# Optimization experiments

Hardware: AMD Instinct MI355X
Metric: run time of the kernel (lower is better)

The kernel has to match this reference:

```python
import jax, jax.numpy as jnp
import numpy as np

NQ = 8    # QCNN qubits
NLQ = 4   # QLSTM qubits == hidden_dim
C64 = jnp.complex64

H_GATE = (1.0 / np.sqrt(2.0)) * jnp.array([[1, 1], [1, -1]], dtype=C64)


def ap1(st, U, q):
    # apply 2x2 gate U on qubit axis q of state st (shape (2,)*n)
    s = jnp.moveaxis(st, q, -1)
    s = jnp.einsum('ij,...j->...i', U, s)
    return jnp.moveaxis(s, -1, q)


def apcx(st, c, t):
    # CNOT with control c, target t: flip target slice where control == 1
    s = jnp.moveaxis(st, (c, t), (-2, -1))
    s = jnp.stack([s[..., 0, :], s[..., 1, ::-1]], axis=-2)
    return jnp.moveaxis(s, (-2, -1), (c, t))


def RX(t):
    c = jnp.cos(t / 2).astype(C64)
    s = (-1j * jnp.sin(t / 2)).astype(C64)
    return jnp.stack([jnp.stack([c, s]), jnp.stack([s, c])])


def RY(t):
    c = jnp.cos(t / 2)
    s = jnp.sin(t / 2)
    return jnp.stack([jnp.stack([c, -s]), jnp.stack([s, c])]).astype(C64)


def RZ(t):
    e = jnp.exp(-0.5j * t).astype(C64)
    z = jnp.zeros((), C64)
    return jnp.stack([jnp.stack([e, z]), jnp.stack([z, jnp.conj(e)])])


def PH(t):
    # qiskit phase gate P(t) = diag(1, e^{i t})
    e = jnp.exp(1j * t).astype(C64)
    o = jnp.ones((), C64)
    z = jnp.zeros((), C64)
    return jnp.stack([jnp.stack([o, z]), jnp.stack([z, e])])


def init_state(n):
    st = jnp.zeros((2,) * n, C64)
    return st.at[(0,) * n].set(1.0)


def zexp(st, q):
    # <Z_q> of statevector st
    p = st.real ** 2 + st.imag ** 2
    m = p.sum(axis=tuple(a for a in range(st.ndim) if a != q))
    return m[0] - m[1]


def conv_block(st, p, q1, q2):
    st = ap1(st, RZ(-np.pi / 2), q2)
    st = apcx(st, q2, q1)
    st = ap1(st, RZ(p[0]), q1)
    st = ap1(st, RY(p[1]), q2)
    st = apcx(st, q1, q2)
    st = ap1(st, RY(p[2]), q2)
    st = apcx(st, q2, q1)
    st = ap1(st, RZ(np.pi / 2), q1)
    return st


def pool_block(st, p, src, sink):
    st = ap1(st, RZ(-np.pi / 2), sink)
    st = apcx(st, sink, src)
    st = ap1(st, RZ(p[0]), src)
    st = ap1(st, RY(p[1]), sink)
    st = apcx(st, src, sink)
    st = ap1(st, RY(p[2]), sink)
    return st


QCNN_SPECS = [
    (conv_block, [(0, 1), (2, 3), (4, 5), (6, 7)]),  # c1
    (pool_block, [(0, 1), (2, 3), (4, 5), (6, 7)]),  # p1
    (conv_block, [(0, 1), (2, 3)]),                  # c2
    (pool_block, [(0, 1), (2, 3)]),                  # p2
    (conv_block, [(0, 1)]),                          # c3
    (pool_block, [(0, 1)]),                          # p3
]


def qcnn_single(x, w):
    # x: (8,) feature angles, w: (42,) ansatz weights
    st = init_state(NQ)
    for _ in range(2):
        for q in range(NQ):
            st = ap1(st, H_GATE, q)
        for q in range(NQ):
            st = ap1(st, PH(2.0 * x[q]), q)
    idx = 0
    for blk, prs in QCNN_SPECS:
        for a, b in prs:
            st = blk(st, w[idx:idx + 3], a, b)
            idx += 3
    return zexp(st, NQ - 1)  # 'ZIIIIIII' => Z on qubit 7 (little-endian)


def qgate_single(v, theta):
    # v: (4,) encoder angles (per sample), theta: (4,) trainable RX angles
    st = init_state(NLQ)
    for i in range(NLQ):
        st = ap1(st, RX(v[i]), i)
    for i in range(NLQ):
        st = ap1(st, RX(theta[i]), i)
    for i in range(NLQ - 1):
        st = apcx(st, i, i + 1)
    st = apcx(st, NLQ - 1, 0)
    return jnp.stack([zexp(st, q) for q in range(NLQ)])


qgate = jax.vmap(qgate_single, in_axes=(0, None))


def setup_inputs() -> dict:
    key = jax.random.key(0)
    ks = jax.random.split(key, 12)
    B, S = 16, 128
    x = jax.random.uniform(ks[0], (B, S, NQ), jnp.float32) * np.pi
    qcnn_w = jax.random.normal(ks[1], (42,), jnp.float32) * 0.1

    def lin(k, out_d, in_d):
        k1, k2 = jax.random.split(k)
        lim = 1.0 / np.sqrt(in_d)
        W = jax.random.uniform(k1, (out_d, in_d), jnp.float32, -lim, lim)
        b = jax.random.uniform(k2, (out_d,), jnp.float32, -lim, lim)
        return W, b

    Wf, bf = lin(ks[2], NLQ, 1 + NLQ)
    Wi, bi = lin(ks[3], NLQ, 1 + NLQ)
    Wg, bg = lin(ks[4], NLQ, 1 + NLQ)
    Wo, bo = lin(ks[5], NLQ, 1 + NLQ)
    theta_f = jax.random.normal(ks[6], (NLQ,), jnp.float32) * 0.1
    theta_i = jax.random.normal(ks[7], (NLQ,), jnp.float32) * 0.1
    theta_g = jax.random.normal(ks[8], (NLQ,), jnp.float32) * 0.1
    theta_o = jax.random.normal(ks[9], (NLQ,), jnp.float32) * 0.1
    Wh, bh = lin(ks[10], 1, NLQ)
    return dict(x=x, qcnn_w=qcnn_w, theta_f=theta_f, theta_i=theta_i,
                theta_g=theta_g, theta_o=theta_o, Wf=Wf, bf=bf, Wi=Wi, bi=bi,
                Wg=Wg, bg=bg, Wo=Wo, bo=bo, Wh=Wh, bh=bh)


def reference(x, qcnn_w, theta_f, theta_i, theta_g, theta_o,
              Wf, bf, Wi, bi, Wg, bg, Wo, bo, Wh, bh):
    B, S, _ = x.shape
    flat = x.reshape(B * S, NQ)
    qcnn_out = jax.vmap(qcnn_single, in_axes=(0, None))(flat, qcnn_w)
    qcnn_out = qcnn_out.reshape(B, S, 1)
    lstm_in = jnp.transpose(qcnn_out, (1, 0, 2))  # (S, B, 1)
    h0 = jnp.zeros((B, NLQ), x.dtype)
    c0 = jnp.zeros((B, NLQ), x.dtype)

    def step(carry, xt):
        hx, cx = carry
        comb = jnp.concatenate([xt, hx], axis=1)  # (B, 1 + hidden)
        f = jax.nn.sigmoid(qgate(comb @ Wf.T + bf, theta_f))
        i = jax.nn.sigmoid(qgate(comb @ Wi.T + bi, theta_i))
        g = jnp.tanh(qgate(comb @ Wg.T + bg, theta_g))
        o = jax.nn.sigmoid(qgate(comb @ Wo.T + bo, theta_o))
        cx = f * cx + i * g
        hx = o * jnp.tanh(cx)
        return (hx, cx), hx

    _, outs = jax.lax.scan(step, (h0, c0), lstm_in)  # outs: (S, B, hidden)
    logits = outs[-1] @ Wh.T + bh  # (B, 1)
    return qcnn_out, logits
```

## Files before the change

kernel.cpp:

```cpp
#include <hip/hip_runtime.h>
#include <math.h>

#define PI_F 3.14159265358979323846f
#define FLAG_MAGIC 0x9E3779B9u

typedef int v2i __attribute__((ext_vector_type(2)));

__device__ __forceinline__ float rcpf(float x) { return __builtin_amdgcn_rcpf(x); }
__device__ __forceinline__ void fswap(float2& p, float2& q) { float2 t = p; p = q; q = t; }


template<int Q>
__device__ __forceinline__ float exq(float v) {
    if constexpr (Q == 2)
        return __int_as_float(__builtin_amdgcn_update_dpp(0, __float_as_int(v), 0xB1, 0xF, 0xF, true));
    else if constexpr (Q == 3)
        return __int_as_float(__builtin_amdgcn_update_dpp(0, __float_as_int(v), 0x4E, 0xF, 0xF, true));
    else if constexpr (Q == 4)
        return __int_as_float(__builtin_amdgcn_ds_swizzle(__float_as_int(v), 0x101F));
    else if constexpr (Q == 5)
        return __int_as_float(__builtin_amdgcn_ds_swizzle(__float_as_int(v), 0x201F));
    else if constexpr (Q == 6)
        return __int_as_float(__builtin_amdgcn_ds_swizzle(__float_as_int(v), 0x401F));
    else {
        v2i r = __builtin_amdgcn_permlane32_swap(__float_as_int(v), __float_as_int(v), false, false);
        return __int_as_float((threadIdx.x & 32) ? r[0] : r[1]);
    }
}

template<int Q>
__device__ __forceinline__ void rzg(float2 a[4], float th, int lane) {
    float c = __cosf(0.5f * th), s = __sinf(0.5f * th);
    if constexpr (Q >= 2) {
        float se = ((lane >> (Q - 2)) & 1) ? s : -s;
        #pragma unroll
        for (int r = 0; r < 4; ++r) {
            float nx = c * a[r].x - se * a[r].y;
            float ny = c * a[r].y + se * a[r].x;
            a[r] = make_float2(nx, ny);
        }
    } else {
        #pragma unroll
        for (int r = 0; r < 4; ++r) {
            int bit = (Q == 0) ? (r >> 1) : (r & 1);
            float se = bit ? s : -s;
            float nx = c * a[r].x - se * a[r].y;
            float ny = c * a[r].y + se * a[r].x;
            a[r] = make_float2(nx, ny);
        }
    }
}

template<int Q>
__device__ __forceinline__ void ryg(float2 a[4], float th, int lane) {
    float c = __cosf(0.5f * th), s = __sinf(0.5f * th);
    if constexpr (Q >= 2) {
        float se = ((lane >> (Q - 2)) & 1) ? s : -s;
        #pragma unroll
        for (int r = 0; r < 4; ++r) {
            float ox = exq<Q>(a[r].x), oy = exq<Q>(a[r].y);
            a[r] = make_float2(c * a[r].x + se * ox, c * a[r].y + se * oy);
        }
    } else if constexpr (Q == 0) {
        #pragma unroll
        for (int r = 0; r < 2; ++r) {
            float2 lo = a[r], hi = a[r + 2];
            a[r]     = make_float2(c * lo.x - s * hi.x, c * lo.y - s * hi.y);
            a[r + 2] = make_float2(s * lo.x + c * hi.x, s * lo.y + c * hi.y);
        }
    } else {
        #pragma unroll
        for (int r = 0; r < 4; r += 2) {
            float2 lo = a[r], hi = a[r + 1];
            a[r]     = make_float2(c * lo.x - s * hi.x, c * lo.y - s * hi.y);
            a[r + 1] = make_float2(s * lo.x + c * hi.x, s * lo.y + c * hi.y);
        }
    }
}

template<int C, int T>
__device__ __forceinline__ void cxg(float2 a[4], int lane) {
    if constexpr (C >= 2) {
        bool cb = (lane >> (C - 2)) & 1;
        #pragma unroll
        for (int r = 0; r < 4; ++r) {
            float ox = exq<T>(a[r].x), oy = exq<T>(a[r].y);
            a[r].x = cb ? ox : a[r].x;
            a[r].y = cb ? oy : a[r].y;
        }
    } else if constexpr (C == 0 && T == 1) {
        fswap(a[2], a[3]);
    } else {
        fswap(a[1], a[3]);
    }
}

template<int Q>
__device__ __forceinline__ void featg(float2 a[4], float xq, int lane) {
    float phi = 2.0f * xq;
    float e1x = __cosf(phi), e1y = __sinf(phi);
    float e2x = e1x * e1x - e1y * e1y;
    float e2y = 2.0f * e1x * e1y;
    float2 u00 = make_float2(0.5f * (1.0f + e1x),  0.5f * e1y);
    float2 u01 = make_float2(0.5f * (1.0f - e1x), -0.5f * e1y);
    float2 u10 = make_float2(0.5f * (e1x - e2x), 0.5f * (e1y - e2y));
    float2 u11 = make_float2(0.5f * (e1x + e2x), 0.5f * (e1y + e2y));
    if constexpr (Q >= 2) {
        bool bset = (lane >> (Q - 2)) & 1;
        float csx = bset ? u11.x : u00.x, csy = bset ? u11.y : u00.y;
        float cox = bset ? u10.x : u01.x, coy = bset ? u10.y : u01.y;
        #pragma unroll
        for (int r = 0; r < 4; ++r) {
            float ox = exq<Q>(a[r].x), oy = exq<Q>(a[r].y);
            float nx = csx * a[r].x - csy * a[r].y + cox * ox - coy * oy;
            float ny = csx * a[r].y + csy * a[r].x + cox * oy + coy * ox;
            a[r] = make_float2(nx, ny);
        }
    } else {
        float2 l, h;
        #define APPL(LO, HI)                                                        \
            l = a[LO]; h = a[HI];                                                   \
            a[LO] = make_float2(u00.x*l.x - u00.y*l.y + u01.x*h.x - u01.y*h.y,      \
                                u00.x*l.y + u00.y*l.x + u01.x*h.y + u01.y*h.x);     \
            a[HI] = make_float2(u10.x*l.x - u10.y*l.y + u11.x*h.x - u11.y*h.y,      \
                                u10.x*l.y + u10.y*l.x + u11.x*h.y + u11.y*h.x);
        if constexpr (Q == 0) { APPL(0, 2) APPL(1, 3) }
        else                  { APPL(0, 1) APPL(2, 3) }
        #undef APPL
    }
}

template<int Q1, int Q2>
__device__ __forceinline__ void convg(float2 a[4], const float* __restrict__ p, int lane) {
    rzg<Q2>(a, -0.5f * PI_F, lane);
    cxg<Q2, Q1>(a, lane);
    rzg<Q1>(a, p[0], lane);
    ryg<Q2>(a, p[1], lane);
    cxg<Q1, Q2>(a, lane);
    ryg<Q2>(a, p[2], lane);
    cxg<Q2, Q1>(a, lane);
    rzg<Q1>(a, 0.5f * PI_F, lane);
}

template<int Q1, int Q2>
__device__ __forceinline__ void poolg(float2 a[4], const float* __restrict__ p, int lane) {
    rzg<Q2>(a, -0.5f * PI_F, lane);
    cxg<Q2, Q1>(a, lane);
    rzg<Q1>(a, p[0], lane);
    ryg<Q2>(a, p[1], lane);
    cxg<Q1, Q2>(a, lane);
    ryg<Q2>(a, p[2], lane);
}

template<int CTRL>
__device__ __forceinline__ float bq(float v) {
    return __int_as_float(__builtin_amdgcn_update_dpp(0, __float_as_int(v), CTRL, 0xF, 0xF, true));
}

__device__ __forceinline__ float pick4(bool b0, bool b1, float a0, float a1, float a2, float a3) {
    float t01 = b0 ? a1 : a0;
    float t23 = b0 ? a3 : a2;
    return b1 ? t23 : t01;
}


__global__ __launch_bounds__(256) void fused_kernel(
    const float* __restrict__ x,  const float* __restrict__ w,
    const float* __restrict__ thf, const float* __restrict__ thi,
    const float* __restrict__ thg, const float* __restrict__ tho,
    const float* __restrict__ Wf, const float* __restrict__ bf,
    const float* __restrict__ Wi, const float* __restrict__ bi,
    const float* __restrict__ Wg, const float* __restrict__ bg,
    const float* __restrict__ Wo, const float* __restrict__ bo,
    const float* __restrict__ Wh, const float* __restrict__ bh,
    float* __restrict__ out, unsigned long long* __restrict__ flg) {
    __shared__ __align__(16) float qsh[16 * 132];
    int lane = threadIdx.x & 63;
    int wave = threadIdx.x >> 6;
    unsigned* epoch = (unsigned*)(flg + 2048);

    if (blockIdx.x != 512) {
        unsigned key = FLAG_MAGIC ^ __hip_atomic_load(epoch, __ATOMIC_RELAXED, __HIP_MEMORY_SCOPE_AGENT);
        int n = blockIdx.x * 4 + wave;
        float2 a[4];
        a[0] = make_float2(lane == 0 ? 1.0f : 0.0f, 0.0f);
        a[1] = make_float2(0.0f, 0.0f);
        a[2] = make_float2(0.0f, 0.0f);
        a[3] = make_float2(0.0f, 0.0f);

        const float* xr = x + n * 8;
        featg<0>(a, xr[0], lane);
        featg<1>(a, xr[1], lane);
        featg<2>(a, xr[2], lane);
        featg<3>(a, xr[3], lane);
        featg<4>(a, xr[4], lane);
        featg<5>(a, xr[5], lane);
        featg<6>(a, xr[6], lane);
        featg<7>(a, xr[7], lane);

        convg<0,1>(a, w + 0,  lane);
        convg<2,3>(a, w + 3,  lane);
        convg<4,5>(a, w + 6,  lane);
        convg<6,7>(a, w + 9,  lane);
        poolg<0,1>(a, w + 12, lane);
        poolg<2,3>(a, w + 15, lane);
        poolg<4,5>(a, w + 18, lane);
        poolg<6,7>(a, w + 21, lane);
        convg<0,1>(a, w + 24, lane);
        convg<2,3>(a, w + 27, lane);
        poolg<0,1>(a, w + 30, lane);
        poolg<2,3>(a, w + 33, lane);
        convg<0,1>(a, w + 36, lane);
        poolg<0,1>(a, w + 39, lane);

        float ssum = 0.f;
        #pragma unroll
        for (int r = 0; r < 4; ++r)
            ssum += a[r].x * a[r].x + a[r].y * a[r].y;
        ssum = (lane & 32) ? -ssum : ssum;
        ssum += exq<2>(ssum);
        ssum += exq<3>(ssum);
        ssum += exq<4>(ssum);
        ssum += exq<5>(ssum);
        ssum += exq<6>(ssum);
        {
            v2i rr = __builtin_amdgcn_permlane32_swap(__float_as_int(ssum), __float_as_int(ssum), false, false);
            ssum = __int_as_float((threadIdx.x & 32) ? rr[0] : rr[1]) +
                   __int_as_float((threadIdx.x & 32) ? rr[1] : rr[0]);
        }
        if (lane == 0) {
            out[n] = ssum;
            unsigned long long pk = ((unsigned long long)__float_as_uint(ssum) << 32)
                                  | (unsigned long long)key;
            __hip_atomic_store(&flg[n], pk, __ATOMIC_RELAXED, __HIP_MEMORY_SCOPE_AGENT);
        }
        return;
    }

    if (wave != 0) return;
    unsigned key = FLAG_MAGIC ^ __hip_atomic_load(epoch, __ATOMIC_RELAXED, __HIP_MEMORY_SCOPE_AGENT);

    for (int j = 0; j < 32; ++j) {
        int idx = j * 64 + lane;
        unsigned long long v;
        do {
            v = __hip_atomic_load(&flg[idx], __ATOMIC_RELAXED, __HIP_MEMORY_SCOPE_AGENT);
        } while ((unsigned)v != key);
        qsh[(idx >> 7) * 132 + (idx & 127)] = __uint_as_float((unsigned)(v >> 32));
    }
    __builtin_amdgcn_wave_barrier();

    int b = lane >> 2, q = lane & 3;
    bool qb0 = q & 1, qb1 = q & 2;
    const float* Wp = (q == 0) ? Wf : (q == 1) ? Wi : (q == 2) ? Wg : Wo;
    const float* bp = (q == 0) ? bf : (q == 1) ? bi : (q == 2) ? bg : bo;
    const float* tp = (q == 0) ? thf : (q == 1) ? thi : (q == 2) ? thg : tho;

    float W[20], av[4];
    #pragma unroll
    for (int k = 0; k < 20; ++k) W[k] = Wp[k];
    #pragma unroll
    for (int r = 0; r < 4; ++r) av[r] = bp[r] + tp[r];

    float nA = (q == 2) ? 1.0f : 0.0f;
    float nB = (q == 2) ? -2.0f : 1.0f;
    float nK = (q == 2) ? 2.0f : -1.0f;

    float c = 0.f;
    float h0 = 0.f, h1 = 0.f, h2 = 0.f, h3 = 0.f;
    const float* qrow = &qsh[b * 132];
    float xv = qrow[0];

    for (int t = 0; t < 128; ++t) {
        float xn = qrow[t + 1];
        float vA = av[0] + W[0]*xv  + W[1]*h0  + W[2]*h1  + W[3]*h2  + W[4]*h3;
        float vB = av[1] + W[5]*xv  + W[6]*h0  + W[7]*h1  + W[8]*h2  + W[9]*h3;
        float vC = av[2] + W[10]*xv + W[11]*h0 + W[12]*h1 + W[13]*h2 + W[14]*h3;
        float vD = av[3] + W[15]*xv + W[16]*h0 + W[17]*h1 + W[18]*h2 + W[19]*h3;
        float cA = __cosf(vA), cB = __cosf(vB), cC = __cosf(vC), cD = __cosf(vD);
        float r1 = cA * cB, r2 = r1 * cC, r3 = r2 * cD, r0 = cB * (cC * cD);
        float E0 = __expf(nK * r0), E1 = __expf(nK * r1);
        float E2 = __expf(nK * r2), E3 = __expf(nK * r3);
        float n0 = nA + nB * rcpf(E0 + 1.0f);
        float n1 = nA + nB * rcpf(E1 + 1.0f);
        float n2 = nA + nB * rcpf(E2 + 1.0f);
        float n3 = nA + nB * rcpf(E3 + 1.0f);
        float F0 = bq<0x00>(n0), F1 = bq<0x00>(n1), F2 = bq<0x00>(n2), F3 = bq<0x00>(n3);
        float I0 = bq<0x55>(n0), I1 = bq<0x55>(n1), I2 = bq<0x55>(n2), I3 = bq<0x55>(n3);
        float G0 = bq<0xAA>(n0), G1 = bq<0xAA>(n1), G2 = bq<0xAA>(n2), G3 = bq<0xAA>(n3);
        float O0 = bq<0xFF>(n0), O1 = bq<0xFF>(n1), O2 = bq<0xFF>(n2), O3 = bq<0xFF>(n3);
        float F = pick4(qb0, qb1, F0, F1, F2, F3);
        float I = pick4(qb0, qb1, I0, I1, I2, I3);
        float G = pick4(qb0, qb1, G0, G1, G2, G3);
        float O = pick4(qb0, qb1, O0, O1, O2, O3);
        c = F * c + I * G;
        float Ec = __expf(2.0f * c);
        float tau = 1.0f - 2.0f * rcpf(Ec + 1.0f);
        float hq = O * tau;
        h0 = bq<0x00>(hq);
        h1 = bq<0x55>(hq);
        h2 = bq<0xAA>(hq);
        h3 = bq<0xFF>(hq);
        xv = xn;
    }

    if (q == 0)
        out[2048 + b] = bh[0] + Wh[0]*h0 + Wh[1]*h1 + Wh[2]*h2 + Wh[3]*h3;

    if (lane == 0)
        __hip_atomic_fetch_add(epoch, 1u, __ATOMIC_RELAXED, __HIP_MEMORY_SCOPE_AGENT);
}

extern "C" void kernel_launch(void* const* d_in, const int* in_sizes, int n_in,
                              void* d_out, int out_size, void* d_ws, size_t ws_size,
                              hipStream_t stream) {
    fused_kernel<<<513, 256, 0, stream>>>(
        (const float*)d_in[0],  (const float*)d_in[1],
        (const float*)d_in[2],  (const float*)d_in[3],
        (const float*)d_in[4],  (const float*)d_in[5],
        (const float*)d_in[6],  (const float*)d_in[7],
        (const float*)d_in[8],  (const float*)d_in[9],
        (const float*)d_in[10], (const float*)d_in[11],
        (const float*)d_in[12], (const float*)d_in[13],
        (const float*)d_in[14], (const float*)d_in[15],
        (float*)d_out, (unsigned long long*)d_ws);
}
```

Before: 129.3 us.

## Overlap LSTM recurrence with QCNN production via timestep-major flag ordering

QCNN work items are remapped so that flag index n is timestep-major (batch = n&15, t = n>>4). The LSTM wave can then consume 64-entry chunks covering four timesteps for all 16 batches as soon as they are ready, instead of waiting for all 2048 flags before starting the recurrence. Polling now uses s_sleep and is interleaved with the sequential scan loop. The risk is that the recurrence stalls whenever producer blocks are late, and that launch_bounds(256,1) changes occupancy for the QCNN blocks.

New measurement: 122.6 us. 1.05x faster.

```diff
diff --git a/kernel.cpp b/kernel.cpp
--- a/kernel.cpp
+++ b/kernel.cpp
@@ -164,7 +164,19 @@
 }
 
 
-__global__ __launch_bounds__(256) void fused_kernel(
+__device__ __forceinline__ void stage_chunk(int m, int lane, unsigned key,
+                                            unsigned long long* __restrict__ flg,
+                                            float* qsh) {
+    int idx = m * 64 + lane;
+    unsigned long long v = __hip_atomic_load(&flg[idx], __ATOMIC_RELAXED, __HIP_MEMORY_SCOPE_AGENT);
+    while ((unsigned)v != key) {
+        __builtin_amdgcn_s_sleep(1);
+        v = __hip_atomic_load(&flg[idx], __ATOMIC_RELAXED, __HIP_MEMORY_SCOPE_AGENT);
+    }
+    qsh[(idx & 15) * 132 + (idx >> 4)] = __uint_as_float((unsigned)(v >> 32));
+}
+
+__global__ __launch_bounds__(256, 1) void fused_kernel(
     const float* __restrict__ x,  const float* __restrict__ w,
     const float* __restrict__ thf, const float* __restrict__ thi,
     const float* __restrict__ thg, const float* __restrict__ tho,
@@ -182,13 +194,15 @@
     if (blockIdx.x != 512) {
         unsigned key = FLAG_MAGIC ^ __hip_atomic_load(epoch, __ATOMIC_RELAXED, __HIP_MEMORY_SCOPE_AGENT);
         int n = blockIdx.x * 4 + wave;
+        int bb = n & 15, tt = n >> 4;
+        int sidx = bb * 128 + tt;
         float2 a[4];
         a[0] = make_float2(lane == 0 ? 1.0f : 0.0f, 0.0f);
         a[1] = make_float2(0.0f, 0.0f);
         a[2] = make_float2(0.0f, 0.0f);
         a[3] = make_float2(0.0f, 0.0f);
 
-        const float* xr = x + n * 8;
+        const float* xr = x + sidx * 8;
         featg<0>(a, xr[0], lane);
         featg<1>(a, xr[1], lane);
         featg<2>(a, xr[2], lane);
@@ -229,7 +243,7 @@
                    __int_as_float((threadIdx.x & 32) ? rr[1] : rr[0]);
         }
         if (lane == 0) {
-            out[n] = ssum;
+            out[sidx] = ssum;
             unsigned long long pk = ((unsigned long long)__float_as_uint(ssum) << 32)
                                   | (unsigned long long)key;
             __hip_atomic_store(&flg[n], pk, __ATOMIC_RELAXED, __HIP_MEMORY_SCOPE_AGENT);
@@ -240,14 +254,7 @@
     if (wave != 0) return;
     unsigned key = FLAG_MAGIC ^ __hip_atomic_load(epoch, __ATOMIC_RELAXED, __HIP_MEMORY_SCOPE_AGENT);
 
-    for (int j = 0; j < 32; ++j) {
-        int idx = j * 64 + lane;
-        unsigned long long v;
-        do {
-            v = __hip_atomic_load(&flg[idx], __ATOMIC_RELAXED, __HIP_MEMORY_SCOPE_AGENT);
-        } while ((unsigned)v != key);
-        qsh[(idx >> 7) * 132 + (idx & 127)] = __uint_as_float((unsigned)(v >> 32));
-    }
+    stage_chunk(0, lane, key, flg, qsh);
     __builtin_amdgcn_wave_barrier();
 
     int b = lane >> 2, q = lane & 3;
@@ -269,39 +276,43 @@
     float c = 0.f;
     float h0 = 0.f, h1 = 0.f, h2 = 0.f, h3 = 0.f;
     const float* qrow = &qsh[b * 132];
-    float xv = qrow[0];
-
-    for (int t = 0; t < 128; ++t) {
-        float xn = qrow[t + 1];
-        float vA = av[0] + W[0]*xv  + W[1]*h0  + W[2]*h1  + W[3]*h2  + W[4]*h3;
-        float vB = av[1] + W[5]*xv  + W[6]*h0  + W[7]*h1  + W[8]*h2  + W[9]*h3;
-        float vC = av[2] + W[10]*xv + W[11]*h0 + W[12]*h1 + W[13]*h2 + W[14]*h3;
-        float vD = av[3] + W[15]*xv + W[16]*h0 + W[17]*h1 + W[18]*h2 + W[19]*h3;
-        float cA = __cosf(vA), cB = __cosf(vB), cC = __cosf(vC), cD = __cosf(vD);
-        float r1 = cA * cB, r2 = r1 * cC, r3 = r2 * cD, r0 = cB * (cC * cD);
-        float E0 = __expf(nK * r0), E1 = __expf(nK * r1);
-        float E2 = __expf(nK * r2), E3 = __expf(nK * r3);
-        float n0 = nA + nB * rcpf(E0 + 1.0f);
-        float n1 = nA + nB * rcpf(E1 + 1.0f);
-        float n2 = nA + nB * rcpf(E2 + 1.0f);
-        float n3 = nA + nB * rcpf(E3 + 1.0f);
-        float F0 = bq<0x00>(n0), F1 = bq<0x00>(n1), F2 = bq<0x00>(n2), F3 = bq<0x00>(n3);
-        float I0 = bq<0x55>(n0), I1 = bq<0x55>(n1), I2 = bq<0x55>(n2), I3 = bq<0x55>(n3);
-        float G0 = bq<0xAA>(n0), G1 = bq<0xAA>(n1), G2 = bq<0xAA>(n2), G3 = bq<0xAA>(n3);
-        float O0 = bq<0xFF>(n0), O1 = bq<0xFF>(n1), O2 = bq<0xFF>(n2), O3 = bq<0xFF>(n3);
-        float F = pick4(qb0, qb1, F0, F1, F2, F3);
-        float I = pick4(qb0, qb1, I0, I1, I2, I3);
-        float G = pick4(qb0, qb1, G0, G1, G2, G3);
-        float O = pick4(qb0, qb1, O0, O1, O2, O3);
-        c = F * c + I * G;
-        float Ec = __expf(2.0f * c);
-        float tau = 1.0f - 2.0f * rcpf(Ec + 1.0f);
-        float hq = O * tau;
-        h0 = bq<0x00>(hq);
-        h1 = bq<0x55>(hq);
-        h2 = bq<0xAA>(hq);
-        h3 = bq<0xFF>(hq);
-        xv = xn;
+
+    for (int j = 0; j < 32; ++j) {
+        if (j < 31) stage_chunk(j + 1, lane, key, flg, qsh);
+        __builtin_amdgcn_wave_barrier();
+        #pragma unroll
+        for (int k = 0; k < 4; ++k) {
+            int t = 4 * j + k;
+            float xv = qrow[t];
+            float vA = av[0] + W[0]*xv  + W[1]*h0  + W[2]*h1  + W[3]*h2  + W[4]*h3;
+            float vB = av[1] + W[5]*xv  + W[6]*h0  + W[7]*h1  + W[8]*h2  + W[9]*h3;
+            float vC = av[2] + W[10]*xv + W[11]*h0 + W[12]*h1 + W[13]*h2 + W[14]*h3;
+            float vD = av[3] + W[15]*xv + W[16]*h0 + W[17]*h1 + W[18]*h2 + W[19]*h3;
+            float cA = __cosf(vA), cB = __cosf(vB), cC = __cosf(vC), cD = __cosf(vD);
+            float r1 = cA * cB, r2 = r1 * cC, r3 = r2 * cD, r0 = cB * (cC * cD);
+            float E0 = __expf(nK * r0), E1 = __expf(nK * r1);
+            float E2 = __expf(nK * r2), E3 = __expf(nK * r3);
+            float n0 = nA + nB * rcpf(E0 + 1.0f);
+            float n1 = nA + nB * rcpf(E1 + 1.0f);
+            float n2 = nA + nB * rcpf(E2 + 1.0f);
+            float n3 = nA + nB * rcpf(E3 + 1.0f);
+            float F0 = bq<0x00>(n0), F1 = bq<0x00>(n1), F2 = bq<0x00>(n2), F3 = bq<0x00>(n3);
+            float I0 = bq<0x55>(n0), I1 = bq<0x55>(n1), I2 = bq<0x55>(n2), I3 = bq<0x55>(n3);
+            float G0 = bq<0xAA>(n0), G1 = bq<0xAA>(n1), G2 = bq<0xAA>(n2), G3 = bq<0xAA>(n3);
+            float O0 = bq<0xFF>(n0), O1 = bq<0xFF>(n1), O2 = bq<0xFF>(n2), O3 = bq<0xFF>(n3);
+            float F = pick4(qb0, qb1, F0, F1, F2, F3);
+            float I = pick4(qb0, qb1, I0, I1, I2, I3);
+            float G = pick4(qb0, qb1, G0, G1, G2, G3);
+            float O = pick4(qb0, qb1, O0, O1, O2, O3);
+            c = F * c + I * G;
+            float Ec = __expf(2.0f * c);
+            float tau = 1.0f - 2.0f * rcpf(Ec + 1.0f);
+            float hq = O * tau;
+            h0 = bq<0x00>(hq);
+            h1 = bq<0x55>(hq);
+            h2 = bq<0xAA>(hq);
+            h3 = bq<0xFF>(hq);
+        }
     }
 
     if (q == 0)
```
